# Optimization experiments

Measured on AMD Instinct MI355X. Metric: run time of the kernel, lower is better.

Reference implementation:

```python
import jax, jax.numpy as jnp
import numpy as np

B, S, H, QIN, RIN = 32, 8192, 256, 256, 256
TANH_EXPLORATION = 10.0


def setup_inputs() -> dict:
    key = jax.random.key(0)
    ks = jax.random.split(key, 7)
    bound = 1.0 / np.sqrt(H)
    return {
        "query": jax.random.normal(ks[0], (B, QIN), dtype=jnp.float32),
        "ref": jax.random.normal(ks[1], (S, B, RIN), dtype=jnp.float32),
        # nn.Linear(QIN, H): weight [H, QIN], bias [H]
        "Wq": jax.random.normal(ks[2], (H, QIN), dtype=jnp.float32) * (1.0 / np.sqrt(QIN)),
        "bq": jax.random.normal(ks[3], (H,), dtype=jnp.float32) * 0.01,
        # nn.Conv1d(RIN, H, kernel=1): equivalent to a pointwise linear, weight [H, RIN], bias [H]
        "Wr": jax.random.normal(ks[4], (H, RIN), dtype=jnp.float32) * (1.0 / np.sqrt(RIN)),
        "br": jax.random.normal(ks[5], (H,), dtype=jnp.float32) * 0.01,
        "v": jax.random.uniform(ks[6], (H,), dtype=jnp.float32, minval=-bound, maxval=bound),
    }


def reference(query, ref, Wq, bq, Wr, br, v):
    # ref: [S, B, RIN] -> permute(1,2,0) -> [B, RIN, S]
    ref_p = jnp.transpose(ref, (1, 2, 0))
    # project_query: [B, H]
    q = query @ Wq.T + bq
    # project_ref (1x1 conv == pointwise linear over channel dim): e [B, H, S]
    e = jnp.einsum("hr,brs->bhs", Wr, ref_p) + br[None, :, None]
    # u[b,s] = sum_h v[h] * tanh(q[b,h] + e[b,h,s])
    u = jnp.einsum("h,bhs->bs", v, jnp.tanh(q[:, :, None] + e))
    # use_tanh=True path
    return e, TANH_EXPLORATION * jnp.tanh(u)
```

## Files before the change

kernel.cpp:

```cpp
#include <hip/hip_runtime.h>

#define NB 32
#define NS 8192
#define NH 256
#define NR 256
#define NQ 256

typedef __bf16 bf16x8 __attribute__((ext_vector_type(8)));
typedef float  f32x4  __attribute__((ext_vector_type(4)));

__device__ __forceinline__ float fast_tanh(float x) {
  x = fminf(15.0f, fmaxf(-15.0f, x));
  float e = __expf(2.0f * x);
  return (e - 1.0f) * __builtin_amdgcn_rcpf(e + 1.0f);
}

__device__ __forceinline__ void split8(float4 a, float4 b, bf16x8& hi, bf16x8& lo) {
  float x[8] = {a.x, a.y, a.z, a.w, b.x, b.y, b.z, b.w};
#pragma unroll
  for (int j = 0; j < 8; ++j) {
    __bf16 h = (__bf16)x[j];
    hi[j] = h;
    lo[j] = (__bf16)(x[j] - (float)h);
  }
}

__global__ __launch_bounds__(256) void prep_kernel(
    const float* __restrict__ query, const float* __restrict__ Wq,
    const float* __restrict__ bq, const float* __restrict__ Wr,
    float* __restrict__ ws_q, __bf16* __restrict__ wsAhi, __bf16* __restrict__ wsAlo) {
  const int tid = threadIdx.x;
  const int blk = blockIdx.x;
  if (blk < NB) {
    const float4* qr = reinterpret_cast<const float4*>(query + blk * NQ);
    const float4* wr = reinterpret_cast<const float4*>(Wq + tid * NQ);
    float acc = 0.0f;
#pragma unroll 8
    for (int i = 0; i < NQ / 4; ++i) {
      float4 a = qr[i], w = wr[i];
      acc += a.x * w.x + a.y * w.y + a.z * w.z + a.w * w.w;
    }
    ws_q[blk * NH + tid] = acc + bq[tid];
  } else {
    const int gid = (blk - NB) * 256 + tid;
    const int l  = gid & 63;
    const int mt = (gid >> 6) & 15;
    const int ks = gid >> 10;
    const int row = 16 * mt + (l & 15);
    const int kb  = 32 * ks + 8 * (l >> 4);
    const float4* src = reinterpret_cast<const float4*>(Wr + row * NR + kb);
    bf16x8 hi, lo;
    split8(src[0], src[1], hi, lo);
    *reinterpret_cast<bf16x8*>(wsAhi + (size_t)gid * 8) = hi;
    *reinterpret_cast<bf16x8*>(wsAlo + (size_t)gid * 8) = lo;
  }
}

__device__ __forceinline__ void barrier_no_vmem_drain() {
  asm volatile("s_waitcnt lgkmcnt(0)" ::: "memory");
  __builtin_amdgcn_sched_barrier(0);
  __builtin_amdgcn_s_barrier();
  __builtin_amdgcn_sched_barrier(0);
}

__global__ __launch_bounds__(256, 2) void attn_kernel(
    const float* __restrict__ ref, const float* __restrict__ br,
    const float* __restrict__ v, const float* __restrict__ ws_q,
    const __bf16* __restrict__ wsAhi, const __bf16* __restrict__ wsAlo,
    float* __restrict__ e_out, float* __restrict__ u_out) {
  __shared__ __bf16 lXhi[2][4 * 64 * 8];
  __shared__ __bf16 lXlo[2][4 * 64 * 8];
  __shared__ float  u_part[4][64];

  const int tid = threadIdx.x;
  const int l   = tid & 63;
  const int wm  = tid >> 6;
  const int s0  = blockIdx.x * 64;
  const int b   = blockIdx.y;

  const float* srcX = ref + (size_t)(s0 + 16 * wm + (l & 15)) * (NB * NR)
                          + (size_t)b * NR + 8 * (l >> 4);

  f32x4 acc[4][4];
  const f32x4 zero = {0.f, 0.f, 0.f, 0.f};
#pragma unroll
  for (int mt = 0; mt < 4; ++mt)
#pragma unroll
    for (int nt = 0; nt < 4; ++nt) acc[mt][nt] = zero;

  float4 xa0 = *reinterpret_cast<const float4*>(srcX + 0);
  float4 xa1 = *reinterpret_cast<const float4*>(srcX + 4);
  float4 xb0 = *reinterpret_cast<const float4*>(srcX + 32);
  float4 xb1 = *reinterpret_cast<const float4*>(srcX + 36);

#pragma unroll 1
  for (int ks = 0; ks < NR / 32; ++ks) {
    const int cur = ks & 1;
    bf16x8 ah[4], al[4];
#pragma unroll
    for (int mt = 0; mt < 4; ++mt) {
      const size_t fo = ((size_t)(ks * 16 + wm * 4 + mt) * 64 + l) * 8;
      ah[mt] = *reinterpret_cast<const bf16x8*>(wsAhi + fo);
      al[mt] = *reinterpret_cast<const bf16x8*>(wsAlo + fo);
    }
    bf16x8 xhi, xlo;
    split8(xa0, xa1, xhi, xlo);
    *reinterpret_cast<bf16x8*>(lXhi[cur] + tid * 8) = xhi;
    *reinterpret_cast<bf16x8*>(lXlo[cur] + tid * 8) = xlo;
    xa0 = xb0; xa1 = xb1;
    if (ks + 2 < NR / 32) {
      xb0 = *reinterpret_cast<const float4*>(srcX + (ks + 2) * 32);
      xb1 = *reinterpret_cast<const float4*>(srcX + (ks + 2) * 32 + 4);
    }
    barrier_no_vmem_drain();

    bf16x8 bh[4], bl[4];
#pragma unroll
    for (int nt = 0; nt < 4; ++nt) {
      bh[nt] = *reinterpret_cast<const bf16x8*>(lXhi[cur] + (nt * 64 + l) * 8);
      bl[nt] = *reinterpret_cast<const bf16x8*>(lXlo[cur] + (nt * 64 + l) * 8);
    }
    __builtin_amdgcn_s_setprio(1);
#pragma unroll
    for (int mt = 0; mt < 4; ++mt) {
#pragma unroll
      for (int nt = 0; nt < 4; ++nt) {
        acc[mt][nt] = __builtin_amdgcn_mfma_f32_16x16x32_bf16(ah[mt], bh[nt], acc[mt][nt], 0, 0, 0);
        acc[mt][nt] = __builtin_amdgcn_mfma_f32_16x16x32_bf16(ah[mt], bl[nt], acc[mt][nt], 0, 0, 0);
        acc[mt][nt] = __builtin_amdgcn_mfma_f32_16x16x32_bf16(al[mt], bh[nt], acc[mt][nt], 0, 0, 0);
      }
    }
    __builtin_amdgcn_s_setprio(0);
  }

  const int col = l & 15;
  const int rq  = l >> 4;
  float psum[4] = {0.f, 0.f, 0.f, 0.f};
#pragma unroll
  for (int mt = 0; mt < 4; ++mt) {
#pragma unroll
    for (int r = 0; r < 4; ++r) {
      const int h = 64 * wm + 16 * mt + 4 * rq + r;
      const float brv = br[h];
      const float qv  = ws_q[b * NH + h];
      const float vv  = v[h];
#pragma unroll
      for (int nt = 0; nt < 4; ++nt) {
        float e = acc[mt][nt][r] + brv;
        e_out[(size_t)b * NH * NS + (size_t)h * NS + (s0 + 16 * nt + col)] = e;
        psum[nt] += vv * fast_tanh(qv + e);
      }
    }
  }
#pragma unroll
  for (int nt = 0; nt < 4; ++nt) {
    float p = psum[nt];
    p += __shfl_xor(p, 16, 64);
    p += __shfl_xor(p, 32, 64);
    if (l < 16) u_part[wm][16 * nt + col] = p;
  }
  barrier_no_vmem_drain();
  if (tid < 64) {
    float u = u_part[0][tid] + u_part[1][tid] + u_part[2][tid] + u_part[3][tid];
    u_out[(size_t)b * NS + s0 + tid] = 10.0f * fast_tanh(u);
  }
}

extern "C" void kernel_launch(void* const* d_in, const int* in_sizes, int n_in,
                              void* d_out, int out_size, void* d_ws, size_t ws_size,
                              hipStream_t stream) {
  const float* query = (const float*)d_in[0];
  const float* ref   = (const float*)d_in[1];
  const float* Wq    = (const float*)d_in[2];
  const float* bq    = (const float*)d_in[3];
  const float* Wr    = (const float*)d_in[4];
  const float* br    = (const float*)d_in[5];
  const float* v     = (const float*)d_in[6];

  float* e_out = (float*)d_out;
  float* u_out = e_out + (size_t)NB * NH * NS;

  float*  ws_q  = (float*)d_ws;
  __bf16* wsAhi = (__bf16*)((char*)d_ws + 32 * 1024);
  __bf16* wsAlo = (__bf16*)((char*)d_ws + 32 * 1024 + 128 * 1024);

  prep_kernel<<<dim3(NB + 32), 256, 0, stream>>>(query, Wq, bq, Wr, ws_q, wsAhi, wsAlo);
  attn_kernel<<<dim3(NS / 64, NB), 256, 0, stream>>>(ref, br, v, ws_q, wsAhi, wsAlo, e_out, u_out);
}
```

Before: 188.1 us.

## Load ref tiles directly into registers per wave, dropping LDS staging and barrier

Each wave now reads all four N tiles of ref straight from global memory and splits them to bf16 hi/lo in registers, instead of the block cooperatively staging them through double-buffered LDS with a barrier. The aim is to remove LDS traffic and per-iteration synchronisation, and the launch bound is raised to three blocks per CU. In exchange, every wave re-reads the same ref data, multiplying global/L2 load traffic by four and adding register pressure.

```diff
diff --git a/kernel.cpp b/kernel.cpp
--- a/kernel.cpp
+++ b/kernel.cpp
@@ -63,14 +63,12 @@
   __builtin_amdgcn_sched_barrier(0);
 }
 
-__global__ __launch_bounds__(256, 2) void attn_kernel(
+__global__ __launch_bounds__(256, 3) void attn_kernel(
     const float* __restrict__ ref, const float* __restrict__ br,
     const float* __restrict__ v, const float* __restrict__ ws_q,
     const __bf16* __restrict__ wsAhi, const __bf16* __restrict__ wsAlo,
     float* __restrict__ e_out, float* __restrict__ u_out) {
-  __shared__ __bf16 lXhi[2][4 * 64 * 8];
-  __shared__ __bf16 lXlo[2][4 * 64 * 8];
-  __shared__ float  u_part[4][64];
+  __shared__ float u_part[4][64];
 
   const int tid = threadIdx.x;
   const int l   = tid & 63;
@@ -78,8 +76,10 @@
   const int s0  = blockIdx.x * 64;
   const int b   = blockIdx.y;
 
-  const float* srcX = ref + (size_t)(s0 + 16 * wm + (l & 15)) * (NB * NR)
-                          + (size_t)b * NR + 8 * (l >> 4);
+  const float* pB0 = ref + (size_t)(s0 + 0  + (l & 15)) * (NB * NR) + (size_t)b * NR + 8 * (l >> 4);
+  const float* pB1 = pB0 + (size_t)16 * NB * NR;
+  const float* pB2 = pB1 + (size_t)16 * NB * NR;
+  const float* pB3 = pB2 + (size_t)16 * NB * NR;
 
   f32x4 acc[4][4];
   const f32x4 zero = {0.f, 0.f, 0.f, 0.f};
@@ -88,14 +88,14 @@
 #pragma unroll
     for (int nt = 0; nt < 4; ++nt) acc[mt][nt] = zero;
 
-  float4 xa0 = *reinterpret_cast<const float4*>(srcX + 0);
-  float4 xa1 = *reinterpret_cast<const float4*>(srcX + 4);
-  float4 xb0 = *reinterpret_cast<const float4*>(srcX + 32);
-  float4 xb1 = *reinterpret_cast<const float4*>(srcX + 36);
+  float4 pb[4][2];
+  pb[0][0] = *(const float4*)(pB0); pb[0][1] = *(const float4*)(pB0 + 4);
+  pb[1][0] = *(const float4*)(pB1); pb[1][1] = *(const float4*)(pB1 + 4);
+  pb[2][0] = *(const float4*)(pB2); pb[2][1] = *(const float4*)(pB2 + 4);
+  pb[3][0] = *(const float4*)(pB3); pb[3][1] = *(const float4*)(pB3 + 4);
 
 #pragma unroll 1
   for (int ks = 0; ks < NR / 32; ++ks) {
-    const int cur = ks & 1;
     bf16x8 ah[4], al[4];
 #pragma unroll
     for (int mt = 0; mt < 4; ++mt) {
@@ -103,23 +103,15 @@
       ah[mt] = *reinterpret_cast<const bf16x8*>(wsAhi + fo);
       al[mt] = *reinterpret_cast<const bf16x8*>(wsAlo + fo);
     }
-    bf16x8 xhi, xlo;
-    split8(xa0, xa1, xhi, xlo);
-    *reinterpret_cast<bf16x8*>(lXhi[cur] + tid * 8) = xhi;
-    *reinterpret_cast<bf16x8*>(lXlo[cur] + tid * 8) = xlo;
-    xa0 = xb0; xa1 = xb1;
-    if (ks + 2 < NR / 32) {
-      xb0 = *reinterpret_cast<const float4*>(srcX + (ks + 2) * 32);
-      xb1 = *reinterpret_cast<const float4*>(srcX + (ks + 2) * 32 + 4);
-    }
-    barrier_no_vmem_drain();
-
     bf16x8 bh[4], bl[4];
 #pragma unroll
-    for (int nt = 0; nt < 4; ++nt) {
-      bh[nt] = *reinterpret_cast<const bf16x8*>(lXhi[cur] + (nt * 64 + l) * 8);
-      bl[nt] = *reinterpret_cast<const bf16x8*>(lXlo[cur] + (nt * 64 + l) * 8);
-    }
+    for (int nt = 0; nt < 4; ++nt) split8(pb[nt][0], pb[nt][1], bh[nt], bl[nt]);
+    const int kn = (ks < NR / 32 - 1) ? (ks + 1) * 32 : ks * 32;
+    pb[0][0] = *(const float4*)(pB0 + kn); pb[0][1] = *(const float4*)(pB0 + kn + 4);
+    pb[1][0] = *(const float4*)(pB1 + kn); pb[1][1] = *(const float4*)(pB1 + kn + 4);
+    pb[2][0] = *(const float4*)(pB2 + kn); pb[2][1] = *(const float4*)(pB2 + kn + 4);
+    pb[3][0] = *(const float4*)(pB3 + kn); pb[3][1] = *(const float4*)(pB3 + kn + 4);
+
     __builtin_amdgcn_s_setprio(1);
 #pragma unroll
     for (int mt = 0; mt < 4; ++mt) {
```

Measured after the change: 471.7 us. 151% more time.
